# Optimization experiments

Hardware: AMD Instinct MI355X
Metric: run time of the kernel (lower is better)

## Reference

```python
import jax, jax.numpy as jnp
import numpy as np

V = 32000   # vocab.size
E = 512     # embed_dim
H = 512     # hidden_dim
L = 2       # num_layers
W = 32      # window_size
S = 512     # seq_len
B = 8       # batch


def setup_inputs() -> dict:
    key = jax.random.key(0)
    ks = jax.random.split(key, 2 + 4 * L)
    bound = 1.0 / np.sqrt(H)
    inp = {
        "encoder_input": jax.random.randint(ks[0], (S, B), 0, V),
        "embed_table": jax.random.normal(ks[1], (V, E), jnp.float32),
    }
    for l in range(L):
        in_dim = E if l == 0 else H
        k = ks[2 + 4 * l: 6 + 4 * l]
        inp[f"w_ih_{l}"] = jax.random.uniform(k[0], (4 * H, in_dim), jnp.float32, -bound, bound)
        inp[f"w_hh_{l}"] = jax.random.uniform(k[1], (4 * H, H), jnp.float32, -bound, bound)
        inp[f"b_ih_{l}"] = jax.random.uniform(k[2], (4 * H,), jnp.float32, -bound, bound)
        inp[f"b_hh_{l}"] = jax.random.uniform(k[3], (4 * H,), jnp.float32, -bound, bound)
    return inp


def _lstm_layer(x, mask, w_ih, w_hh, b_ih, b_hh):
    # x: [T, N, D]; mask: [T, N, 1]. Masked steps keep (h, c), so every window
    # effectively starts from a zero state at its first valid position (same as
    # running a fresh LSTM on each window, torch gate order i,f,g,o).
    N = x.shape[1]
    Hd = w_hh.shape[1]
    bias = b_ih + b_hh

    def step(carry, inp_):
        h, c = carry
        xt, mt = inp_
        gates = xt @ w_ih.T + h @ w_hh.T + bias  # [N, 4H]
        i, f, g, o = jnp.split(gates, 4, axis=-1)
        i = jax.nn.sigmoid(i)
        f = jax.nn.sigmoid(f)
        g = jnp.tanh(g)
        o = jax.nn.sigmoid(o)
        c_new = f * c + i * g
        h_new = o * jnp.tanh(c_new)
        h = jnp.where(mt, h_new, h)
        c = jnp.where(mt, c_new, c)
        return (h, c), h

    z = jnp.zeros((N, Hd), x.dtype)
    (h, _), ys = jax.lax.scan(step, (z, z), (x, mask))
    return ys, h


def reference(encoder_input, embed_table,
              w_ih_0, w_hh_0, b_ih_0, b_hh_0,
              w_ih_1, w_hh_1, b_ih_1, b_hh_1):
    emb = embed_table[encoder_input]              # [S, B, E]
    T = W + 1
    # window position t for target index i is i - W + t (invalid when < 0)
    pos = jnp.arange(S)[None, :] - W + jnp.arange(T)[:, None]  # [T, S]
    valid = pos >= 0
    windows = emb[jnp.clip(pos, 0)]               # [T, S, B, E]
    x = windows.reshape(T, S * B, E)
    mask = jnp.broadcast_to(valid[:, :, None], (T, S, B)).reshape(T, S * B, 1)

    params = [(w_ih_0, w_hh_0, b_ih_0, b_hh_0), (w_ih_1, w_hh_1, b_ih_1, b_hh_1)]
    h = None
    for (wi, wh, bi, bh) in params:
        x, h = _lstm_layer(x, mask, wi, wh, bi, bh)
    # original takes encoder_output at the last window position == final hidden
    return h.reshape(S, B, H)
```

## Files before the change

### kernel.cpp

```cpp
#include <hip/hip_runtime.h>
#include <stdint.h>

#define NROWS 4096
#define HDIM  512
#define GDIM  2048
#define WWIN  32

typedef __attribute__((ext_vector_type(8))) short short8;
typedef __attribute__((ext_vector_type(4))) float f32x4;

__device__ __forceinline__ unsigned short f2bf(float x){
  union { float f; unsigned int u; } v; v.f = x;
  unsigned int u = v.u + 0x7fffu + ((v.u >> 16) & 1u);
  return (unsigned short)(u >> 16);
}

__device__ __forceinline__ void gld16(const void* g, void* l){
  __builtin_amdgcn_global_load_lds(
      (const __attribute__((address_space(1))) unsigned int*)g,
      (__attribute__((address_space(3))) unsigned int*)l, 16, 0, 0);
}

__device__ __forceinline__ float sigm(float x){ return 1.f/(1.f + __expf(-x)); }
__device__ __forceinline__ float tanh_f(float x){ return 1.f - 2.f/(1.f + __expf(2.f*x)); }

__device__ __forceinline__ void gemm_tile_db(
    const char* A0, const char* A1, const char* Bsrc,
    int ldbB, int nk, int r0, int c0,
    char* smem, int wr, int wc, int lane, f32x4 acc[4][4])
{
  const int tid = threadIdx.x;
  const int oo0 = tid * 16;
  const int srow = oo0 >> 7;
  const int scb  = oo0 & 127;
  const size_t aOff = (size_t)(r0 + srow) * 1024 + scb;
  const size_t bOff = (size_t)(c0 + srow) * (size_t)ldbB + scb;

  auto STAGE = [&](int kk, int buf){
    const char* Ap = (kk < 8) ? A0 : A1;
    const size_t kbA = (size_t)(kk & 7) * 128;
    const size_t kbB = (size_t)kk * 128;
    char* AsB = smem + buf * 16384;
    char* BsB = smem + 32768 + buf * 16384;
    #pragma unroll
    for (int i = 0; i < 4; ++i){
      const size_t rstep = (size_t)i * 32;
      gld16(Ap   + aOff + rstep * 1024          + kbA, AsB + i*4096 + oo0);
      gld16(Bsrc + bOff + rstep * (size_t)ldbB  + kbB, BsB + i*4096 + oo0);
    }
  };

  STAGE(0, 0);
  __syncthreads();

  const int lr = lane & 15;
  const int lk = (lane >> 4) * 8;

  for (int kk = 0; kk < nk; ++kk){
    const int cur = kk & 1;
    if (kk + 1 < nk) STAGE(kk + 1, cur ^ 1);

    const unsigned short* As = (const unsigned short*)(smem + cur*16384);
    const unsigned short* Bs = (const unsigned short*)(smem + 32768 + cur*16384);
    short8 a[2][4], b[2][4];
    #pragma unroll
    for (int h = 0; h < 2; ++h){
      const int k32 = h * 32;
      #pragma unroll
      for (int m = 0; m < 4; ++m)
        a[h][m] = *(const short8*)(As + (64*wr + 16*m + lr)*64 + k32 + lk);
      #pragma unroll
      for (int n = 0; n < 4; ++n)
        b[h][n] = *(const short8*)(Bs + (64*wc + 16*n + lr)*64 + k32 + lk);
    }
    __builtin_amdgcn_s_setprio(1);
    #pragma unroll
    for (int h = 0; h < 2; ++h)
      #pragma unroll
      for (int m = 0; m < 4; ++m)
        #pragma unroll
        for (int n = 0; n < 4; ++n)
          acc[m][n] = __builtin_amdgcn_mfma_f32_16x16x32_bf16(a[h][m], b[h][n], acc[m][n], 0, 0, 0);
    __builtin_amdgcn_s_setprio(0);

    __syncthreads();
  }
}

__global__ void __launch_bounds__(256) prep_weights(
    const float* wih0, const float* whh0, const float* bih0, const float* bhh0,
    const float* wih1, const float* whh1, const float* bih1, const float* bhh1,
    unsigned short* BrIh0, unsigned short* Br0, unsigned short* Br1,
    float* bias0r, float* br1)
{
  const int j = blockIdx.x;
  const int g = j & 3, hd = j >> 2;
  const int r = g*512 + hd;
  for (int k = threadIdx.x; k < 512; k += 256){
    BrIh0[(size_t)j*512 + k]      = f2bf(wih0[(size_t)r*512 + k]);
    Br0  [(size_t)j*512 + k]      = f2bf(whh0[(size_t)r*512 + k]);
    Br1  [(size_t)j*1024 + k]     = f2bf(wih1[(size_t)r*512 + k]);
    Br1  [(size_t)j*1024 + 512+k] = f2bf(whh1[(size_t)r*512 + k]);
  }
  if (threadIdx.x == 0){
    bias0r[j] = bih0[r] + bhh0[r];
    br1[j]    = bih1[r] + bhh1[r];
  }
}

__global__ void __launch_bounds__(256) gather_embed(const int* enc, const float* tbl,
                                                    unsigned short* E)
{
  const int n = blockIdx.x;
  const int idx = enc[n];
  const float* src = tbl + (size_t)idx * 512;
  unsigned short* dst = E + (size_t)n * 512;
  for (int e = threadIdx.x; e < 512; e += 256) dst[e] = f2bf(src[e]);
}

__global__ void __launch_bounds__(256) p0_gemm(const unsigned short* E,
                                               const unsigned short* BrIh0,
                                               const float* bias0r, float* P0)
{
  __shared__ __align__(16) char smem[65536];
  const int tid  = threadIdx.x;
  const int lane = tid & 63, wid = tid >> 6;
  const int wr = wid >> 1, wc = wid & 1;
  const int bid = blockIdx.x;
  const int r0 = (bid >> 4) * 128, c0 = (bid & 15) * 128;
  f32x4 acc[4][4] = {};
  gemm_tile_db((const char*)E, nullptr, (const char*)BrIh0, 1024, 8,
               r0, c0, smem, wr, wc, lane, acc);
  #pragma unroll
  for (int m = 0; m < 4; ++m){
    const int rowb = r0 + 64*wr + 16*m + ((lane >> 4) << 2);
    #pragma unroll
    for (int n = 0; n < 4; ++n){
      const int colb = c0 + 64*wc + 16*n + (lane & 15);
      const float bs = bias0r[colb];
      #pragma unroll
      for (int r = 0; r < 4; ++r)
        P0[(size_t)(rowb + r)*GDIM + colb] = acc[m][n][r] + bs;
    }
  }
}

__global__ void __launch_bounds__(256) step_kernel(
    unsigned short* h0, unsigned short* h1, float* c0b, float* c1b,
    const unsigned short* Br0, const unsigned short* Br1,
    const float* P0, const float* br1, float* out, int tau, int bidOff)
{
  const int bid = blockIdx.x + bidOff;
  const bool L1 = (bid >= 512);
  const int t  = L1 ? (tau - 1) : tau;
  const int pr = (tau + 1) & 1, pw = tau & 1;
  const int lb = L1 ? (bid - 512) : bid;
  const int r0  = (lb >> 4) * 128;
  const int c0v = (lb & 15) * 128;

  __shared__ __align__(16) char smem[65536];
  const int tid  = threadIdx.x;
  const int lane = tid & 63, wid = tid >> 6;
  const int wr = wid >> 1, wc = wid & 1;

  f32x4 acc[4][4] = {};
  const unsigned short* hA0 = h0 + (size_t)pr * (NROWS*HDIM);
  const unsigned short* hA1 = h1 + (size_t)pr * (NROWS*HDIM);
  if (!L1)
    gemm_tile_db((const char*)hA0, nullptr, (const char*)Br0, 1024, 8,
                 r0, c0v, smem, wr, wc, lane, acc);
  else
    gemm_tile_db((const char*)hA0, (const char*)hA1, (const char*)Br1, 2048, 16,
                 r0, c0v, smem, wr, wc, lane, acc);

  float* cbuf = L1 ? c1b : c0b;
  unsigned short* hw = (L1 ? h1 : h0) + (size_t)pw * (NROWS*HDIM);
  const bool finalStep = (L1 && t == 32);
  float* GLDS = (float*)smem;
  const int GST = 68;

  #pragma unroll
  for (int hp = 0; hp < 2; ++hp){
    __syncthreads();
    if (wc == hp){
      #pragma unroll
      for (int m = 0; m < 4; ++m){
        const int rowb = 64*wr + 16*m + ((lane >> 4) << 2);
        #pragma unroll
        for (int n = 0; n < 4; ++n){
          const int colb = 16*n + (lane & 15);
          #pragma unroll
          for (int r = 0; r < 4; ++r)
            GLDS[(rowb + r)*GST + colb] = acc[m][n][r];
        }
      }
    }
    __syncthreads();
    #pragma unroll
    for (int it = 0; it < 8; ++it){
      const int cid = it*256 + tid;
      const int row = cid >> 4;
      const int l   = cid & 15;
      const int rowg = r0 + row;
      const int hd   = (c0v >> 2) + 16*hp + l;
      const int colg = 4*hd;
      float4 gv = *(const float4*)&GLDS[row*GST + 4*l];
      float gi = gv.x, gf = gv.y, gg = gv.z, go = gv.w;
      const int s  = rowg >> 3;
      const int bb = rowg & 7;
      const int pos = s - WWIN + t;
      if (!L1){
        const int p0r = (pos < 0 ? 0 : pos)*8 + bb;
        float4 pv = *(const float4*)&P0[(size_t)p0r*GDIM + colg];
        gi += pv.x; gf += pv.y; gg += pv.z; go += pv.w;
      } else {
        float4 bv = *(const float4*)&br1[colg];
        gi += bv.x; gf += bv.y; gg += bv.z; go += bv.w;
      }
      const size_t sidx = (size_t)rowg*HDIM + hd;
      float cp = cbuf[sidx];
      float i_ = sigm(gi), f_ = sigm(gf), g_ = tanh_f(gg), o_ = sigm(go);
      float cn = f_*cp + i_*g_;
      float hn = o_*tanh_f(cn);
      if (pos < 0){ cn = 0.f; hn = 0.f; }
      cbuf[sidx] = cn;
      if (finalStep) out[sidx] = hn;
      else           hw[sidx]  = f2bf(hn);
    }
  }
}

extern "C" void kernel_launch(void* const* d_in, const int* in_sizes, int n_in,
                              void* d_out, int out_size, void* d_ws, size_t ws_size,
                              hipStream_t stream)
{
  const int*   enc  = (const int*)d_in[0];
  const float* tbl  = (const float*)d_in[1];
  const float* wih0 = (const float*)d_in[2];
  const float* whh0 = (const float*)d_in[3];
  const float* bih0 = (const float*)d_in[4];
  const float* bhh0 = (const float*)d_in[5];
  const float* wih1 = (const float*)d_in[6];
  const float* whh1 = (const float*)d_in[7];
  const float* bih1 = (const float*)d_in[8];
  const float* bhh1 = (const float*)d_in[9];
  float* out = (float*)d_out;

  char* ws = (char*)d_ws;
  size_t off = 0;
  auto alloc = [&](size_t bytes){
    char* p = ws + off; off += (bytes + 255) & ~(size_t)255; return p;
  };
  unsigned short* E     = (unsigned short*)alloc((size_t)NROWS*512*2);
  unsigned short* BrIh0 = (unsigned short*)alloc((size_t)GDIM*512*2);
  unsigned short* Br0   = (unsigned short*)alloc((size_t)GDIM*512*2);
  unsigned short* Br1   = (unsigned short*)alloc((size_t)GDIM*1024*2);
  float* bias0r = (float*)alloc(GDIM*4);
  float* br1    = (float*)alloc(GDIM*4);
  float* P0     = (float*)alloc((size_t)NROWS*GDIM*4);
  unsigned short* h0 = (unsigned short*)alloc((size_t)2*NROWS*HDIM*2);
  unsigned short* h1 = (unsigned short*)alloc((size_t)2*NROWS*HDIM*2);
  float* c0 = (float*)alloc((size_t)NROWS*HDIM*4);
  float* c1 = (float*)alloc((size_t)NROWS*HDIM*4);
  if (off > ws_size) return;

  hipMemsetAsync(h0, 0, (size_t)33554432, stream);

  prep_weights<<<2048, 256, 0, stream>>>(wih0, whh0, bih0, bhh0,
                                         wih1, whh1, bih1, bhh1,
                                         BrIh0, Br0, Br1, bias0r, br1);
  gather_embed<<<4096, 256, 0, stream>>>(enc, tbl, E);
  p0_gemm<<<512, 256, 0, stream>>>(E, BrIh0, bias0r, P0);
  for (int tau = 0; tau <= 33; ++tau){
    const int grid = (tau == 0 || tau == 33) ? 512 : 1024;
    const int boff = (tau == 33) ? 512 : 0;
    step_kernel<<<grid, 256, 0, stream>>>(h0, h1, c0, c1, Br0, Br1,
                                          P0, br1, out, tau, boff);
  }
}
```

Measured before the change: 1.687 ms.

## Enlarge step GEMM tiles to 256x256 with 4-stage LDS pipeline and 512 threads

The per-timestep LSTM GEMM now uses 256x256 output tiles per block with 8 waves and a 4-deep LDS ring, staged through global_load_lds with XOR swizzling and interleaved half-tile MFMA phases. Block IDs are remapped so layer-0 and layer-1 tiles interleave across the grid. Larger tiles raise arithmetic intensity and cut redundant h and weight reads. The cost is far fewer blocks (128-256) on a GPU with many CUs, plus 128KB of dynamic LDS per block, which limits occupancy.

```diff
diff --git a/kernel.cpp b/kernel.cpp
--- a/kernel.cpp
+++ b/kernel.cpp
@@ -145,65 +145,136 @@
   }
 }
 
-__global__ void __launch_bounds__(256) step_kernel(
+__global__ void __launch_bounds__(512, 2) step_kernel(
     unsigned short* h0, unsigned short* h1, float* c0b, float* c1b,
     const unsigned short* Br0, const unsigned short* Br1,
     const float* P0, const float* br1, float* out, int tau, int bidOff)
 {
-  const int bid = blockIdx.x + bidOff;
-  const bool L1 = (bid >= 512);
+  extern __shared__ __align__(16) char smem[];
+
+  const int x = blockIdx.x & 7, kq = blockIdx.x >> 3;
+  int wk;
+  if (gridDim.x == 256) wk = ((kq & 1) << 7) + x * 16 + (kq >> 1);
+  else                  wk = x * 16 + kq;
+  wk += bidOff;
+
+  const bool L1 = (wk >= 128);
   const int t  = L1 ? (tau - 1) : tau;
   const int pr = (tau + 1) & 1, pw = tau & 1;
-  const int lb = L1 ? (bid - 512) : bid;
-  const int r0  = (lb >> 4) * 128;
-  const int c0v = (lb & 15) * 128;
-
-  __shared__ __align__(16) char smem[65536];
+  const int lb = L1 ? (wk - 128) : wk;
+  const int r0  = (lb >> 3) * 256;
+  const int c0v = (lb & 7) * 256;
+
   const int tid  = threadIdx.x;
-  const int lane = tid & 63, wid = tid >> 6;
-  const int wr = wid >> 1, wc = wid & 1;
-
-  f32x4 acc[4][4] = {};
+  const int lane = tid & 63;
+  const int wid  = tid >> 6;
+  const int wm = wid >> 2, wn = wid & 3;
+  const int lr = lane & 15, sl = lane >> 4;
+
   const unsigned short* hA0 = h0 + (size_t)pr * (NROWS*HDIM);
   const unsigned short* hA1 = h1 + (size_t)pr * (NROWS*HDIM);
-  if (!L1)
-    gemm_tile_db((const char*)hA0, nullptr, (const char*)Br0, 1024, 8,
-                 r0, c0v, smem, wr, wc, lane, acc);
-  else
-    gemm_tile_db((const char*)hA0, (const char*)hA1, (const char*)Br1, 2048, 16,
-                 r0, c0v, smem, wr, wc, lane, acc);
-
+  const char* Bp  = (const char*)(L1 ? Br1 : Br0);
+  const int  ldbB = L1 ? 2048 : 1024;
+  const int  nkt  = L1 ? 32 : 16;
+
+  const int srow  = tid >> 2;
+  const int sbyte = ((tid & 3) ^ ((tid >> 3) & 3)) << 4;
+  const int ph    = (sl ^ ((lr >> 1) & 3)) << 4;
+  const int laneA = (wm*128 + lr) * 64 + ph;
+  const int laneB = (wn*64  + lr) * 64 + ph;
+
+  auto STAGE_A = [&](int kt2, int c){
+    const char* Ap; int kB;
+    if (!L1 || kt2 < 16){ Ap = (const char*)hA0; kB = kt2 * 64; }
+    else                { Ap = (const char*)hA1; kB = (kt2 - 16) * 64; }
+    gld16(Ap + (size_t)(r0 + c*128 + srow) * 1024 + kB + sbyte,
+          smem + (size_t)(kt2 & 3) * 32768 + c*8192 + tid*16);
+  };
+  auto STAGE_B = [&](int kt2, int c){
+    gld16(Bp + (size_t)(c0v + c*128 + srow) * (size_t)ldbB + kt2*64 + sbyte,
+          smem + (size_t)(kt2 & 3) * 32768 + 16384 + c*8192 + tid*16);
+  };
+
+  f32x4 acc[8][4] = {};
+
+  STAGE_A(0,0); STAGE_A(0,1); STAGE_B(0,0); STAGE_B(0,1);
+  STAGE_A(1,0); STAGE_A(1,1); STAGE_B(1,0); STAGE_B(1,1);
+  asm volatile("s_waitcnt vmcnt(4)" ::: "memory");
+  __builtin_amdgcn_s_barrier();
+
+  for (int kt = 0; kt < nkt; ++kt){
+    const char* bufp = smem + (size_t)(kt & 3) * 32768;
+    const bool st = (kt + 2) < nkt;
+    short8 a0[4], a1[4], b[4];
+
+    #pragma unroll
+    for (int m = 0; m < 4; ++m) a0[m] = *(const short8*)(bufp + laneA + m*1024);
+    #pragma unroll
+    for (int n = 0; n < 4; ++n) b[n]  = *(const short8*)(bufp + 16384 + laneB + n*1024);
+    if (st){ STAGE_A(kt+2, 0); STAGE_A(kt+2, 1); }
+    __builtin_amdgcn_s_barrier();
+    asm volatile("s_waitcnt lgkmcnt(0)" ::: "memory");
+    __builtin_amdgcn_sched_barrier(0);
+    __builtin_amdgcn_s_setprio(1);
+    #pragma unroll
+    for (int m = 0; m < 4; ++m)
+      #pragma unroll
+      for (int n = 0; n < 4; ++n)
+        acc[m][n] = __builtin_amdgcn_mfma_f32_16x16x32_bf16(a0[m], b[n], acc[m][n], 0, 0, 0);
+    __builtin_amdgcn_s_setprio(0);
+    __builtin_amdgcn_s_barrier();
+
+    #pragma unroll
+    for (int m = 0; m < 4; ++m) a1[m] = *(const short8*)(bufp + laneA + (4+m)*1024);
+    if (st){
+      STAGE_B(kt+2, 0); STAGE_B(kt+2, 1);
+      asm volatile("s_waitcnt vmcnt(4)" ::: "memory");
+    } else {
+      asm volatile("s_waitcnt vmcnt(0)" ::: "memory");
+    }
+    __builtin_amdgcn_s_barrier();
+    asm volatile("s_waitcnt lgkmcnt(0)" ::: "memory");
+    __builtin_amdgcn_sched_barrier(0);
+    __builtin_amdgcn_s_setprio(1);
+    #pragma unroll
+    for (int m = 0; m < 4; ++m)
+      #pragma unroll
+      for (int n = 0; n < 4; ++n)
+        acc[4+m][n] = __builtin_amdgcn_mfma_f32_16x16x32_bf16(a1[m], b[n], acc[4+m][n], 0, 0, 0);
+    __builtin_amdgcn_s_setprio(0);
+    __builtin_amdgcn_s_barrier();
+  }
+
+  float* GLDS = (float*)smem;
+  const int GST = 68;
   float* cbuf = L1 ? c1b : c0b;
   unsigned short* hw = (L1 ? h1 : h0) + (size_t)pw * (NROWS*HDIM);
   const bool finalStep = (L1 && t == 32);
-  float* GLDS = (float*)smem;
-  const int GST = 68;
-
-  #pragma unroll
-  for (int hp = 0; hp < 2; ++hp){
+
+  for (int pass = 0; pass < 4; ++pass){
     __syncthreads();
-    if (wc == hp){
-      #pragma unroll
-      for (int m = 0; m < 4; ++m){
-        const int rowb = 64*wr + 16*m + ((lane >> 4) << 2);
+    if (wn == pass){
+      #pragma unroll
+      for (int m = 0; m < 8; ++m){
+        const int rowb = wm*128 + m*16 + (sl << 2);
         #pragma unroll
         for (int n = 0; n < 4; ++n){
-          const int colb = 16*n + (lane & 15);
+          const int colb = n*16 + lr;
+          const f32x4 v = acc[m][n];
           #pragma unroll
           for (int r = 0; r < 4; ++r)
-            GLDS[(rowb + r)*GST + colb] = acc[m][n][r];
+            GLDS[(rowb + r)*GST + colb] = v[r];
         }
       }
     }
     __syncthreads();
     #pragma unroll
     for (int it = 0; it < 8; ++it){
-      const int cid = it*256 + tid;
+      const int cid = it*512 + tid;
       const int row = cid >> 4;
       const int l   = cid & 15;
       const int rowg = r0 + row;
-      const int hd   = (c0v >> 2) + 16*hp + l;
-      const int colg = 4*hd;
+      const int hd   = (c0v >> 2) + pass*16 + l;
       float4 gv = *(const float4*)&GLDS[row*GST + 4*l];
       float gi = gv.x, gf = gv.y, gg = gv.z, go = gv.w;
       const int s  = rowg >> 3;
@@ -211,10 +282,10 @@
       const int pos = s - WWIN + t;
       if (!L1){
         const int p0r = (pos < 0 ? 0 : pos)*8 + bb;
-        float4 pv = *(const float4*)&P0[(size_t)p0r*GDIM + colg];
+        float4 pv = *(const float4*)&P0[(size_t)p0r*GDIM + 4*hd];
         gi += pv.x; gf += pv.y; gg += pv.z; go += pv.w;
       } else {
-        float4 bv = *(const float4*)&br1[colg];
+        float4 bv = *(const float4*)&br1[4*hd];
         gi += bv.x; gf += bv.y; gg += bv.z; go += bv.w;
       }
       const size_t sidx = (size_t)rowg*HDIM + hd;
@@ -264,6 +335,9 @@
   float* c1 = (float*)alloc((size_t)NROWS*HDIM*4);
   if (off > ws_size) return;
 
+  (void)hipFuncSetAttribute(reinterpret_cast<const void*>(step_kernel),
+                            hipFuncAttributeMaxDynamicSharedMemorySize, 131072);
+
   hipMemsetAsync(h0, 0, (size_t)33554432, stream);
 
   prep_weights<<<2048, 256, 0, stream>>>(wih0, whh0, bih0, bhh0,
@@ -272,9 +346,9 @@
   gather_embed<<<4096, 256, 0, stream>>>(enc, tbl, E);
   p0_gemm<<<512, 256, 0, stream>>>(E, BrIh0, bias0r, P0);
   for (int tau = 0; tau <= 33; ++tau){
-    const int grid = (tau == 0 || tau == 33) ? 512 : 1024;
-    const int boff = (tau == 33) ? 512 : 0;
-    step_kernel<<<grid, 256, 0, stream>>>(h0, h1, c0, c1, Br0, Br1,
-                                          P0, br1, out, tau, boff);
-  }
-}
+    const int grid = (tau == 0 || tau == 33) ? 128 : 256;
+    const int boff = (tau == 33) ? 128 : 0;
+    step_kernel<<<grid, 512, 131072, stream>>>(h0, h1, c0, c1, Br0, Br1,
+                                               P0, br1, out, tau, boff);
+  }
+}
```

After: 1.714 ms. No clear change (+1.6%).
